# Performance work log

Measured on AMD Instinct MI355X. Metric: run time of the kernel, lower is better.

The kernel has to match this reference:

```python
import jax, jax.numpy as jnp
import numpy as np


def _forward(x, conv_w, conv_b, lin_w, lin_b, W_in, conv1d_w, conv1d_b, W_x, W_dt, b_dt, A_log, Dp, W_out, We, be, Wa, ba, Wq, bq):
    B, _, H, Wd = x.shape
    E = conv_w.shape[0]
    # conv stem: Conv2d(k=3, pad=1) -> flatten(2) -> Linear(H*W -> img_size)
    z = jax.lax.conv_general_dilated(x, conv_w, (1, 1), [(1, 1), (1, 1)],
                                     dimension_numbers=('NCHW', 'OIHW', 'NCHW'))
    z = z + conv_b[None, :, None, None]
    z = z.reshape(B, E, H * Wd)                              # [B,E,HW]
    z = jnp.einsum('ben,mn->bem', z, lin_w) + lin_b          # [B,E,L]
    u = z.transpose(2, 0, 1)                                 # [L,B,E]: Mamba sees batch=L, seq=B
    # ---- Mamba block (mamba_ssm reference math) ----
    di = W_in.shape[0] // 2
    xz = u @ W_in.T                                          # [L,seq,2*di]
    xm, zg = xz[..., :di], xz[..., di:]
    K = conv1d_w.shape[-1]
    xc = jax.lax.conv_general_dilated(xm.transpose(0, 2, 1), conv1d_w, (1,), [(K - 1, 0)],
                                      dimension_numbers=('NCH', 'OIH', 'NCH'),
                                      feature_group_count=di)  # causal depthwise conv
    xs = jax.nn.silu((xc + conv1d_b[None, :, None]).transpose(0, 2, 1))  # [L,seq,di]
    dbl = xs @ W_x.T                                         # [L,seq,dt_rank+2S]
    dt_rank = W_dt.shape[1]
    S = A_log.shape[1]
    delta = jax.nn.softplus(dbl[..., :dt_rank] @ W_dt.T + b_dt)          # [L,seq,di]
    Bm = dbl[..., dt_rank:dt_rank + S]                       # [L,seq,S]
    Cm = dbl[..., dt_rank + S:]                              # [L,seq,S]
    A = -jnp.exp(A_log)                                      # [di,S]

    def step(h, t):
        d_t, b_t, c_t, x_t = t                               # [L,di],[L,S],[L,S],[L,di]
        h = jnp.exp(d_t[:, :, None] * A) * h + (d_t * x_t)[:, :, None] * b_t[:, None, :]
        return h, jnp.einsum('lds,ls->ld', h, c_t)

    h0 = jnp.zeros((u.shape[0], di, S), xs.dtype)
    _, ys = jax.lax.scan(step, h0, (delta.transpose(1, 0, 2), Bm.transpose(1, 0, 2),
                                    Cm.transpose(1, 0, 2), xs.transpose(1, 0, 2)))
    y = (ys.transpose(1, 0, 2) + xs * Dp) * jax.nn.silu(zg)  # [L,seq,di]
    out = y @ W_out.T                                        # [L,seq,E]
    feat = out[-1]                                           # [B,E] (last 'mamba batch' row)
    return feat @ We.T + be, feat @ Wa.T + ba, feat @ Wq.T + bq


def setup_inputs() -> dict:
    key = jax.random.key(0)
    ks = jax.random.split(key, 16)
    B, C, IMG, E, S, K = 512, 1, 32, 128, 256, 4
    di, dt_rank = 2 * E, 8
    sc = 0.02
    return {
        'x': jax.random.normal(ks[0], (B, C, IMG, IMG), jnp.float32),
        'conv_w': sc * jax.random.normal(ks[1], (E, C, 3, 3), jnp.float32),
        'conv_b': jnp.zeros((E,), jnp.float32),
        'lin_w': sc * jax.random.normal(ks[2], (IMG, IMG * IMG), jnp.float32),
        'lin_b': jnp.zeros((IMG,), jnp.float32),
        'W_in': sc * jax.random.normal(ks[3], (2 * di, E), jnp.float32),
        'conv1d_w': sc * jax.random.normal(ks[4], (di, 1, K), jnp.float32),
        'conv1d_b': jnp.zeros((di,), jnp.float32),
        'W_x': sc * jax.random.normal(ks[5], (dt_rank + 2 * S, di), jnp.float32),
        'W_dt': sc * jax.random.normal(ks[6], (di, dt_rank), jnp.float32),
        'b_dt': 0.1 * jax.random.normal(ks[7], (di,), jnp.float32),
        'A_log': jnp.log(jnp.broadcast_to(jnp.arange(1, S + 1, dtype=jnp.float32), (di, S))),
        'Dp': jnp.ones((di,), jnp.float32),
        'W_out': sc * jax.random.normal(ks[8], (E, di), jnp.float32),
        'We': sc * jax.random.normal(ks[9], (1, E), jnp.float32),
        'be': jnp.zeros((1,), jnp.float32),
        'Wa': sc * jax.random.normal(ks[10], (3, E), jnp.float32),
        'ba': jnp.zeros((3,), jnp.float32),
        'Wq': sc * jax.random.normal(ks[11], (4, E), jnp.float32),
        'bq': jnp.zeros((4,), jnp.float32),
    }


def reference(x, conv_w, conv_b, lin_w, lin_b, W_in, conv1d_w, conv1d_b, W_x, W_dt, b_dt, A_log, Dp, W_out, We, be, Wa, ba, Wq, bq):
    return _forward(x, conv_w, conv_b, lin_w, lin_b, W_in, conv1d_w, conv1d_b, W_x,
                    W_dt, b_dt, A_log, Dp, W_out, We, be, Wa, ba, Wq, bq)
```

## Files before the change

kernel.cpp:

```cpp
#include <hip/hip_runtime.h>
#include <math.h>

#define BATCH 512
#define E     128
#define DI    256
#define S     256
#define DTR   8
#define KCONV 4
#define JWX   520

__device__ __forceinline__ float silu_f(float v) {
    return v / (1.0f + __expf(-v));
}

__global__ __launch_bounds__(256) void kT_transpose(
    const float* __restrict__ W_in, const float* __restrict__ W_x,
    const float* __restrict__ W_dt, const float* __restrict__ W_out,
    const float* __restrict__ c1w,
    float* __restrict__ W_inT, float* __restrict__ W_xT,
    float* __restrict__ W_dtT, float* __restrict__ W_outT,
    float* __restrict__ c1wT)
{
    const int bid = blockIdx.x;
    const float* src; float* dst; int J, K, j0;
    if (bid < 9)       { src = W_x;   dst = W_xT;   J = JWX; K = DI;  j0 = bid * 64; }
    else if (bid < 17) { src = W_in;  dst = W_inT;  J = 512; K = E;   j0 = (bid - 9) * 64; }
    else if (bid < 19) { src = W_out; dst = W_outT; J = E;   K = DI;  j0 = (bid - 17) * 64; }
    else if (bid < 23) { src = W_dt;  dst = W_dtT;  J = DI;  K = DTR; j0 = (bid - 19) * 64; }
    else               { src = c1w;   dst = c1wT;   J = DI;  K = KCONV; j0 = (bid - 23) * 64; }
    const int j = j0 + (threadIdx.x & 63);
    if (j >= J) return;
    for (int c = threadIdx.x >> 6; c < K; c += 4)
        dst[c * J + j] = src[j * K + c];
}

__global__ __launch_bounds__(256) void k1_conv_lin(
    const float* __restrict__ x, const float* __restrict__ conv_w,
    const float* __restrict__ conv_b, const float* __restrict__ lin_w,
    const float* __restrict__ lin_b, float* __restrict__ u31)
{
    const int b = blockIdx.x;
    const int tid = threadIdx.x;
    __shared__ float lw[1024];
    __shared__ float red[10][4];
    __shared__ float Tsh[10];

    const float4 lv = ((const float4*)(lin_w + 31 * 1024))[tid];
    ((float4*)lw)[tid] = lv;
    __syncthreads();

    float acc[10];
#pragma unroll
    for (int k = 0; k < 10; k++) acc[k] = 0.0f;

    const float4 xv = ((const float4*)(x + (size_t)b * 1024))[tid];
    const int p0 = tid * 4;
    const int h = p0 >> 5, w0 = p0 & 31;
    const float xa[4] = {xv.x, xv.y, xv.z, xv.w};
#pragma unroll
    for (int k = 0; k < 4; k++) {
        const float xval = xa[k];
        const int w = w0 + k;
#pragma unroll
        for (int i = 0; i < 3; i++) {
            const int hh = h - (i - 1);
            if (hh < 0 || hh > 31) continue;
#pragma unroll
            for (int j = 0; j < 3; j++) {
                const int ww = w - (j - 1);
                if (ww < 0 || ww > 31) continue;
                acc[i * 3 + j] += xval * lw[hh * 32 + ww];
            }
        }
    }
    acc[9] = lv.x + lv.y + lv.z + lv.w;

    const int wv = tid >> 6, ln = tid & 63;
#pragma unroll
    for (int k = 0; k < 10; k++) {
#pragma unroll
        for (int m = 1; m < 64; m <<= 1) acc[k] += __shfl_xor(acc[k], m, 64);
    }
    if (ln == 0) {
#pragma unroll
        for (int k = 0; k < 10; k++) red[k][wv] = acc[k];
    }
    __syncthreads();
    if (tid < 10) Tsh[tid] = red[tid][0] + red[tid][1] + red[tid][2] + red[tid][3];
    __syncthreads();

    if (tid < E) {
        const int e = tid;
        float v = lin_b[31] + conv_b[e] * Tsh[9];
#pragma unroll
        for (int k = 0; k < 9; k++) v += conv_w[e * 9 + k] * Tsh[k];
        u31[b * E + e] = v;
    }
}

__global__ __launch_bounds__(256) void k2a_win(
    const float* __restrict__ u31, const float* __restrict__ W_inT,
    float* __restrict__ xm, float* __restrict__ zg)
{
    const int bb = blockIdx.x * 4;
    const int tid = threadIdx.x;
    __shared__ float u[4][E];
    for (int i = tid; i < 4 * E; i += 256) u[i >> 7][i & 127] = u31[bb * E + i];
    __syncthreads();

    const int r = tid >> 6;
    const int j = blockIdx.y * 64 + (tid & 63);
    float a = 0.0f;
#pragma unroll 8
    for (int e = 0; e < E; e++) a += u[r][e] * W_inT[e * 512 + j];
    if (j < 256) xm[(bb + r) * DI + j] = a;
    else         zg[(bb + r) * DI + (j - 256)] = a;
}

__global__ __launch_bounds__(256) void k2b_conv_wx(
    const float* __restrict__ xm, const float* __restrict__ c1wT,
    const float* __restrict__ conv1d_b, const float* __restrict__ W_xT,
    const float* __restrict__ W_dtT, const float* __restrict__ b_dt,
    float* __restrict__ xs_g, float* __restrict__ delta_g,
    float* __restrict__ Bm, float* __restrict__ Cm)
{
    const int bb = blockIdx.x * 4;
    const int g = blockIdx.y;
    const int tid = threadIdx.x;
    __shared__ float xs[4][DI];
    __shared__ float dtin[4][8];

    for (int idx = tid; idx < 4 * DI; idx += 256) {
        const int r = idx >> 8, c = idx & 255;
        const int b = bb + r;
        float a = 0.0f;
#pragma unroll
        for (int k = 0; k < KCONV; k++) {
            const int src = b - 3 + k;
            if (src >= 0) a += xm[src * DI + c] * c1wT[k * DI + c];
        }
        a += conv1d_b[c];
        const float s = silu_f(a);
        xs[r][c] = s;
        if (g == 0) xs_g[b * DI + c] = s;
    }
    __syncthreads();

    const int r = tid >> 6;
    const int j = g * 64 + (tid & 63);
    if (j < JWX) {
        float a = 0.0f;
#pragma unroll 8
        for (int c = 0; c < DI; c++) a += xs[r][c] * W_xT[c * JWX + j];
        const int b = bb + r;
        if (j < DTR)          dtin[r][j] = a;
        else if (j < DTR + S) Bm[b * S + (j - DTR)] = a;
        else                  Cm[b * S + (j - DTR - S)] = a;
    }
    __syncthreads();

    if (g == 0) {
        const int d = tid;
        const float bd = b_dt[d];
#pragma unroll
        for (int r2 = 0; r2 < 4; r2++) {
            float a = bd;
#pragma unroll
            for (int q = 0; q < DTR; q++) a += dtin[r2][q] * W_dtT[q * DI + d];
            const float sp = (a > 20.0f) ? a : log1pf(__expf(a));
            delta_g[(bb + r2) * DI + d] = sp;
        }
    }
}

template <int NCv>
__global__ __launch_bounds__(256) void k3a_local(
    const float* __restrict__ A_log, const float* __restrict__ delta,
    const float* __restrict__ xs, const float* __restrict__ Bm,
    const float* __restrict__ Cm, float* __restrict__ y,
    float* __restrict__ hloc, float* __restrict__ Dchunk)
{
    constexpr int TCv = BATCH / NCv;
    const int tid = threadIdx.x;
    const int wv = tid >> 6, ln = tid & 63;
    const int d = blockIdx.x * 4 + wv;
    const int c = blockIdx.y;
    const int s0 = ln * 4;
    const int t0 = c * TCv;

    const float4 al = *(const float4*)(A_log + d * S + s0);
    float4 A;
    A.x = -__expf(al.x); A.y = -__expf(al.y);
    A.z = -__expf(al.z); A.w = -__expf(al.w);

    float4 h = make_float4(0.f, 0.f, 0.f, 0.f);
    float cd = 0.0f;
    float pr[8];

    for (int tb = 0; tb < TCv; tb += 8) {
#pragma unroll
        for (int i = 0; i < 8; i++) {
            const int tt = t0 + tb + i;
            const float dd = delta[tt * DI + d];
            cd += dd;
            const float u = dd * xs[tt * DI + d];
            const float4 B = *(const float4*)(Bm + tt * S + s0);
            const float4 C = *(const float4*)(Cm + tt * S + s0);
            h.x = __expf(dd * A.x) * h.x + u * B.x;
            h.y = __expf(dd * A.y) * h.y + u * B.y;
            h.z = __expf(dd * A.z) * h.z + u * B.z;
            h.w = __expf(dd * A.w) * h.w + u * B.w;
            pr[i] = h.x * C.x + h.y * C.y + h.z * C.z + h.w * C.w;
        }
#pragma unroll
        for (int i = 0; i < 8; i++) {
#pragma unroll
            for (int m = 1; m < 64; m <<= 1) pr[i] += __shfl_xor(pr[i], m, 64);
        }
        if (ln == 0) {
#pragma unroll
            for (int i = 0; i < 8; i++) y[(t0 + tb + i) * DI + d] = pr[i];
        }
    }

    *(float4*)(hloc + ((size_t)(c * DI + d)) * S + s0) = h;
    if (ln == 0) Dchunk[c * DI + d] = cd;
}

template <int NCv>
__global__ __launch_bounds__(256) void k3b_carry(
    const float* __restrict__ A_log, const float* __restrict__ hloc,
    const float* __restrict__ Dchunk, float* __restrict__ hin)
{
    const int d = blockIdx.x;
    const int s = threadIdx.x;
    const float A = -__expf(A_log[d * S + s]);

    float h = 0.0f;
    float hf = hloc[((size_t)(0 * DI + d)) * S + s];
    float Dc = Dchunk[0 * DI + d];
    for (int c = 1; c < NCv; c++) {
        float hf_n = 0.0f, Dc_n = 0.0f;
        if (c < NCv - 1) {
            hf_n = hloc[((size_t)(c * DI + d)) * S + s];
            Dc_n = Dchunk[c * DI + d];
        }
        h = hf + __expf(A * Dc) * h;
        hin[((size_t)(c * DI + d)) * S + s] = h;
        hf = hf_n; Dc = Dc_n;
    }
}

template <int NCv>
__global__ __launch_bounds__(256) void k3c_fix(
    const float* __restrict__ A_log, const float* __restrict__ delta,
    const float* __restrict__ Cm, const float* __restrict__ hin,
    float* __restrict__ y)
{
    constexpr int TCv = BATCH / NCv;
    const int tid = threadIdx.x;
    const int wv = tid >> 6, ln = tid & 63;
    const int d = blockIdx.x * 4 + wv;
    const int c = blockIdx.y + 1;
    const int s0 = ln * 4;
    const int t0 = c * TCv;

    const float4 al = *(const float4*)(A_log + d * S + s0);
    float4 A;
    A.x = -__expf(al.x); A.y = -__expf(al.y);
    A.z = -__expf(al.z); A.w = -__expf(al.w);

    const float4 hi = *(const float4*)(hin + ((size_t)(c * DI + d)) * S + s0);

    float cd = 0.0f;
    float pr[8];

    for (int tb = 0; tb < TCv; tb += 8) {
#pragma unroll
        for (int i = 0; i < 8; i++) {
            const int tt = t0 + tb + i;
            const float dd = delta[tt * DI + d];
            cd += dd;
            const float4 C = *(const float4*)(Cm + tt * S + s0);
            const float fx = hi.x * __expf(cd * A.x);
            const float fy = hi.y * __expf(cd * A.y);
            const float fz = hi.z * __expf(cd * A.z);
            const float fw = hi.w * __expf(cd * A.w);
            pr[i] = fx * C.x + fy * C.y + fz * C.z + fw * C.w;
        }
#pragma unroll
        for (int i = 0; i < 8; i++) {
#pragma unroll
            for (int m = 1; m < 64; m <<= 1) pr[i] += __shfl_xor(pr[i], m, 64);
        }
        if (ln == 0) {
#pragma unroll
            for (int i = 0; i < 8; i++) {
                const int tt = t0 + tb + i;
                y[tt * DI + d] += pr[i];
            }
        }
    }
}

__global__ __launch_bounds__(256) void k4_heads(
    const float* __restrict__ y, const float* __restrict__ xs,
    const float* __restrict__ Dp, const float* __restrict__ zg,
    const float* __restrict__ W_outT,
    const float* __restrict__ We, const float* __restrict__ be,
    const float* __restrict__ Wa, const float* __restrict__ ba,
    const float* __restrict__ Wq, const float* __restrict__ bq,
    float* __restrict__ out)
{
    const int bb = blockIdx.x * 2;
    const int tid = threadIdx.x;
    __shared__ float yf[2][DI];
    __shared__ float feat[2][E];

    for (int idx = tid; idx < 2 * DI; idx += 256) {
        const int r = idx >> 8, c = idx & 255;
        const int b = bb + r;
        const float z = zg[b * DI + c];
        yf[r][c] = (y[b * DI + c] + xs[b * DI + c] * Dp[c]) * silu_f(z);
    }
    __syncthreads();

    {
        const int r = tid >> 7, e = tid & 127;
        float a = 0.0f;
#pragma unroll 8
        for (int dd = 0; dd < DI; dd++) a += yf[r][dd] * W_outT[dd * E + e];
        feat[r][e] = a;
    }
    __syncthreads();

    if (tid < 16) {
        const int r = tid >> 3, hd = tid & 7;
        const int b = bb + r;
        const float* wrow;
        float bias;
        int dst;
        if (hd == 0)      { wrow = We;                 bias = be[0];      dst = b; }
        else if (hd < 4)  { wrow = Wa + (hd - 1) * E;  bias = ba[hd - 1]; dst = 512 + b * 3 + (hd - 1); }
        else              { wrow = Wq + (hd - 4) * E;  bias = bq[hd - 4]; dst = 2048 + b * 4 + (hd - 4); }
        float a = bias;
#pragma unroll 4
        for (int e = 0; e < E; e++) a += feat[r][e] * wrow[e];
        out[dst] = a;
    }
}

template <int NCv>
static void launch_scan(const float* A_log, const float* delta, const float* xs,
                        const float* Bm, const float* Cm, float* y,
                        float* hloc, float* hin, float* Dchunk, hipStream_t stream)
{
    k3a_local<NCv><<<dim3(64, NCv), 256, 0, stream>>>(A_log, delta, xs, Bm, Cm, y, hloc, Dchunk);
    k3b_carry<NCv><<<256, 256, 0, stream>>>(A_log, hloc, Dchunk, hin);
    k3c_fix<NCv><<<dim3(64, NCv - 1), 256, 0, stream>>>(A_log, delta, Cm, hin, y);
}

extern "C" void kernel_launch(void* const* d_in, const int* in_sizes, int n_in,
                              void* d_out, int out_size, void* d_ws, size_t ws_size,
                              hipStream_t stream)
{
    const float* x        = (const float*)d_in[0];
    const float* conv_w   = (const float*)d_in[1];
    const float* conv_b   = (const float*)d_in[2];
    const float* lin_w    = (const float*)d_in[3];
    const float* lin_b    = (const float*)d_in[4];
    const float* W_in     = (const float*)d_in[5];
    const float* conv1d_w = (const float*)d_in[6];
    const float* conv1d_b = (const float*)d_in[7];
    const float* W_x      = (const float*)d_in[8];
    const float* W_dt     = (const float*)d_in[9];
    const float* b_dt     = (const float*)d_in[10];
    const float* A_log    = (const float*)d_in[11];
    const float* Dp       = (const float*)d_in[12];
    const float* W_out    = (const float*)d_in[13];
    const float* We       = (const float*)d_in[14];
    const float* be       = (const float*)d_in[15];
    const float* Wa       = (const float*)d_in[16];
    const float* ba       = (const float*)d_in[17];
    const float* Wq       = (const float*)d_in[18];
    const float* bq       = (const float*)d_in[19];
    float* out = (float*)d_out;

    float* ws = (float*)d_ws;
    float* u31   = ws;
    float* xm    = u31 + 512 * 128;
    float* zg    = xm  + 512 * 256;
    float* xs    = zg  + 512 * 256;
    float* delta = xs  + 512 * 256;
    float* Bm    = delta + 512 * 256;
    float* Cm    = Bm  + 512 * 256;
    float* y     = Cm  + 512 * 256;
    float* W_inT = y   + 512 * 256;
    float* W_xT  = W_inT + 128 * 512;
    float* W_dtT = W_xT  + 256 * JWX;
    float* W_outT= W_dtT + 8 * 256;
    float* c1wT  = W_outT+ 256 * 128;
    float* tail  = c1wT  + 4 * 256;

    const size_t base_floats = (size_t)(tail - ws);

    kT_transpose<<<27, 256, 0, stream>>>(W_in, W_x, W_dt, W_out, conv1d_w,
                                         W_inT, W_xT, W_dtT, W_outT, c1wT);
    k1_conv_lin<<<512, 256, 0, stream>>>(x, conv_w, conv_b, lin_w, lin_b, u31);
    k2a_win<<<dim3(128, 8), 256, 0, stream>>>(u31, W_inT, xm, zg);
    k2b_conv_wx<<<dim3(128, 9), 256, 0, stream>>>(xm, c1wT, conv1d_b, W_xT, W_dtT, b_dt,
                                                  xs, delta, Bm, Cm);

    const size_t avail = ws_size / 4 - base_floats;
    if (avail >= (size_t)2 * 32 * DI * S + 32 * DI) {
        float* hloc = tail;
        float* hin  = hloc + (size_t)32 * DI * S;
        float* Dch  = hin  + (size_t)32 * DI * S;
        launch_scan<32>(A_log, delta, xs, Bm, Cm, y, hloc, hin, Dch, stream);
    } else if (avail >= (size_t)2 * 16 * DI * S + 16 * DI) {
        float* hloc = tail;
        float* hin  = hloc + (size_t)16 * DI * S;
        float* Dch  = hin  + (size_t)16 * DI * S;
        launch_scan<16>(A_log, delta, xs, Bm, Cm, y, hloc, hin, Dch, stream);
    } else {
        float* hloc = tail;
        float* hin  = hloc + (size_t)8 * DI * S;
        float* Dch  = hin  + (size_t)8 * DI * S;
        launch_scan<8>(A_log, delta, xs, Bm, Cm, y, hloc, hin, Dch, stream);
    }

    k4_heads<<<256, 256, 0, stream>>>(y, xs, Dp, zg, W_outT, We, be, Wa, ba, Wq, bq, out);
}
```

Before: 185.3 us.

## Fuse pre-kernels, merge W_in with conv/W_x, and fold carry scan into fix

Merges the weight-transpose and conv stem into one launch, and fuses the W_in projection with the causal conv and W_x projection into a single kernel. That kernel recomputes the three halo rows of xm in shared memory instead of writing xm to global. The separate inter-chunk carry kernel is removed; each fix block instead recomputes its incoming state by serially combining prior chunk states, so later chunks do redundant work. This cuts launch count and global traffic, but k2_fused now runs only 128 blocks, down from 1024 and 1152, which lowers parallelism.

```diff
diff --git a/kernel.cpp b/kernel.cpp
--- a/kernel.cpp
+++ b/kernel.cpp
@@ -13,7 +13,10 @@
     return v / (1.0f + __expf(-v));
 }
 
-__global__ __launch_bounds__(256) void kT_transpose(
+__global__ __launch_bounds__(256) void kA_pre(
+    const float* __restrict__ x, const float* __restrict__ conv_w,
+    const float* __restrict__ conv_b, const float* __restrict__ lin_w,
+    const float* __restrict__ lin_b, float* __restrict__ u31,
     const float* __restrict__ W_in, const float* __restrict__ W_x,
     const float* __restrict__ W_dt, const float* __restrict__ W_out,
     const float* __restrict__ c1w,
@@ -21,26 +24,23 @@
     float* __restrict__ W_dtT, float* __restrict__ W_outT,
     float* __restrict__ c1wT)
 {
-    const int bid = blockIdx.x;
-    const float* src; float* dst; int J, K, j0;
-    if (bid < 9)       { src = W_x;   dst = W_xT;   J = JWX; K = DI;  j0 = bid * 64; }
-    else if (bid < 17) { src = W_in;  dst = W_inT;  J = 512; K = E;   j0 = (bid - 9) * 64; }
-    else if (bid < 19) { src = W_out; dst = W_outT; J = E;   K = DI;  j0 = (bid - 17) * 64; }
-    else if (bid < 23) { src = W_dt;  dst = W_dtT;  J = DI;  K = DTR; j0 = (bid - 19) * 64; }
-    else               { src = c1w;   dst = c1wT;   J = DI;  K = KCONV; j0 = (bid - 23) * 64; }
-    const int j = j0 + (threadIdx.x & 63);
-    if (j >= J) return;
-    for (int c = threadIdx.x >> 6; c < K; c += 4)
-        dst[c * J + j] = src[j * K + c];
-}
-
-__global__ __launch_bounds__(256) void k1_conv_lin(
-    const float* __restrict__ x, const float* __restrict__ conv_w,
-    const float* __restrict__ conv_b, const float* __restrict__ lin_w,
-    const float* __restrict__ lin_b, float* __restrict__ u31)
-{
+    const int tid = threadIdx.x;
+    if (blockIdx.x >= 512) {
+        const int bid = blockIdx.x - 512;
+        const float* src; float* dst; int J, K, j0;
+        if (bid < 9)       { src = W_x;   dst = W_xT;   J = JWX; K = DI;    j0 = bid * 64; }
+        else if (bid < 17) { src = W_in;  dst = W_inT;  J = 512; K = E;     j0 = (bid - 9) * 64; }
+        else if (bid < 19) { src = W_out; dst = W_outT; J = E;   K = DI;    j0 = (bid - 17) * 64; }
+        else if (bid < 23) { src = W_dt;  dst = W_dtT;  J = DI;  K = DTR;   j0 = (bid - 19) * 64; }
+        else               { src = c1w;   dst = c1wT;   J = DI;  K = KCONV; j0 = (bid - 23) * 64; }
+        const int j = j0 + (tid & 63);
+        if (j >= J) return;
+        for (int c = tid >> 6; c < K; c += 4)
+            dst[c * J + j] = src[j * K + c];
+        return;
+    }
+
     const int b = blockIdx.x;
-    const int tid = threadIdx.x;
     __shared__ float lw[1024];
     __shared__ float red[10][4];
     __shared__ float Tsh[10];
@@ -98,77 +98,94 @@
     }
 }
 
-__global__ __launch_bounds__(256) void k2a_win(
+__global__ __launch_bounds__(256) void k2_fused(
     const float* __restrict__ u31, const float* __restrict__ W_inT,
-    float* __restrict__ xm, float* __restrict__ zg)
+    const float* __restrict__ c1wT, const float* __restrict__ conv1d_b,
+    const float* __restrict__ W_xT, const float* __restrict__ W_dtT,
+    const float* __restrict__ b_dt,
+    float* __restrict__ zg, float* __restrict__ xs_g,
+    float* __restrict__ delta_g, float* __restrict__ Bm, float* __restrict__ Cm)
 {
     const int bb = blockIdx.x * 4;
     const int tid = threadIdx.x;
-    __shared__ float u[4][E];
-    for (int i = tid; i < 4 * E; i += 256) u[i >> 7][i & 127] = u31[bb * E + i];
-    __syncthreads();
-
-    const int r = tid >> 6;
-    const int j = blockIdx.y * 64 + (tid & 63);
-    float a = 0.0f;
-#pragma unroll 8
-    for (int e = 0; e < E; e++) a += u[r][e] * W_inT[e * 512 + j];
-    if (j < 256) xm[(bb + r) * DI + j] = a;
-    else         zg[(bb + r) * DI + (j - 256)] = a;
-}
-
-__global__ __launch_bounds__(256) void k2b_conv_wx(
-    const float* __restrict__ xm, const float* __restrict__ c1wT,
-    const float* __restrict__ conv1d_b, const float* __restrict__ W_xT,
-    const float* __restrict__ W_dtT, const float* __restrict__ b_dt,
-    float* __restrict__ xs_g, float* __restrict__ delta_g,
-    float* __restrict__ Bm, float* __restrict__ Cm)
-{
-    const int bb = blockIdx.x * 4;
-    const int g = blockIdx.y;
-    const int tid = threadIdx.x;
-    __shared__ float xs[4][DI];
-    __shared__ float dtin[4][8];
+    __shared__ float u[7][E];
+    __shared__ float xmL[7][DI];
+    __shared__ float xsL[4][DI];
+    __shared__ float dt_in[4][8];
+
+    for (int idx = tid; idx < 7 * E; idx += 256) {
+        const int row = idx / E, e = idx - row * E;
+        const int b = bb - 3 + row;
+        u[row][e] = (b >= 0) ? u31[b * E + e] : 0.0f;
+    }
+    __syncthreads();
+
+    {
+        const int c = tid;
+        float xmAcc[7], zgAcc[4];
+#pragma unroll
+        for (int r = 0; r < 7; r++) xmAcc[r] = 0.0f;
+#pragma unroll
+        for (int r = 0; r < 4; r++) zgAcc[r] = 0.0f;
+#pragma unroll 4
+        for (int e = 0; e < E; e++) {
+            const float w0 = W_inT[e * 512 + c];
+            const float w1 = W_inT[e * 512 + 256 + c];
+#pragma unroll
+            for (int r = 0; r < 7; r++) xmAcc[r] += w0 * u[r][e];
+#pragma unroll
+            for (int r = 0; r < 4; r++) zgAcc[r] += w1 * u[3 + r][e];
+        }
+#pragma unroll
+        for (int r = 0; r < 7; r++) xmL[r][c] = xmAcc[r];
+#pragma unroll
+        for (int r = 0; r < 4; r++) zg[(bb + r) * DI + c] = zgAcc[r];
+    }
+    __syncthreads();
 
     for (int idx = tid; idx < 4 * DI; idx += 256) {
         const int r = idx >> 8, c = idx & 255;
-        const int b = bb + r;
         float a = 0.0f;
 #pragma unroll
-        for (int k = 0; k < KCONV; k++) {
-            const int src = b - 3 + k;
-            if (src >= 0) a += xm[src * DI + c] * c1wT[k * DI + c];
-        }
+        for (int k = 0; k < KCONV; k++)
+            a += xmL[r + k][c] * c1wT[k * DI + c];
         a += conv1d_b[c];
         const float s = silu_f(a);
-        xs[r][c] = s;
-        if (g == 0) xs_g[b * DI + c] = s;
-    }
-    __syncthreads();
-
-    const int r = tid >> 6;
-    const int j = g * 64 + (tid & 63);
-    if (j < JWX) {
-        float a = 0.0f;
-#pragma unroll 8
-        for (int c = 0; c < DI; c++) a += xs[r][c] * W_xT[c * JWX + j];
-        const int b = bb + r;
-        if (j < DTR)          dtin[r][j] = a;
-        else if (j < DTR + S) Bm[b * S + (j - DTR)] = a;
-        else                  Cm[b * S + (j - DTR - S)] = a;
-    }
-    __syncthreads();
-
-    if (g == 0) {
+        xsL[r][c] = s;
+        xs_g[(bb + r) * DI + c] = s;
+    }
+    __syncthreads();
+
+    for (int j = tid; j < JWX; j += 256) {
+        float acc[4];
+#pragma unroll
+        for (int r = 0; r < 4; r++) acc[r] = 0.0f;
+#pragma unroll 4
+        for (int c = 0; c < DI; c++) {
+            const float w = W_xT[c * JWX + j];
+#pragma unroll
+            for (int r = 0; r < 4; r++) acc[r] += w * xsL[r][c];
+        }
+#pragma unroll
+        for (int r = 0; r < 4; r++) {
+            const int b = bb + r;
+            if (j < DTR)          dt_in[r][j] = acc[r];
+            else if (j < DTR + S) Bm[b * S + (j - DTR)] = acc[r];
+            else                  Cm[b * S + (j - DTR - S)] = acc[r];
+        }
+    }
+    __syncthreads();
+
+    {
         const int d = tid;
         const float bd = b_dt[d];
 #pragma unroll
-        for (int r2 = 0; r2 < 4; r2++) {
+        for (int r = 0; r < 4; r++) {
             float a = bd;
 #pragma unroll
-            for (int q = 0; q < DTR; q++) a += dtin[r2][q] * W_dtT[q * DI + d];
+            for (int q = 0; q < DTR; q++) a += dt_in[r][q] * W_dtT[q * DI + d];
             const float sp = (a > 20.0f) ? a : log1pf(__expf(a));
-            delta_g[(bb + r2) * DI + d] = sp;
+            delta_g[(bb + r) * DI + d] = sp;
         }
     }
 }
@@ -228,34 +245,10 @@
 }
 
 template <int NCv>
-__global__ __launch_bounds__(256) void k3b_carry(
-    const float* __restrict__ A_log, const float* __restrict__ hloc,
-    const float* __restrict__ Dchunk, float* __restrict__ hin)
-{
-    const int d = blockIdx.x;
-    const int s = threadIdx.x;
-    const float A = -__expf(A_log[d * S + s]);
-
-    float h = 0.0f;
-    float hf = hloc[((size_t)(0 * DI + d)) * S + s];
-    float Dc = Dchunk[0 * DI + d];
-    for (int c = 1; c < NCv; c++) {
-        float hf_n = 0.0f, Dc_n = 0.0f;
-        if (c < NCv - 1) {
-            hf_n = hloc[((size_t)(c * DI + d)) * S + s];
-            Dc_n = Dchunk[c * DI + d];
-        }
-        h = hf + __expf(A * Dc) * h;
-        hin[((size_t)(c * DI + d)) * S + s] = h;
-        hf = hf_n; Dc = Dc_n;
-    }
-}
-
-template <int NCv>
 __global__ __launch_bounds__(256) void k3c_fix(
     const float* __restrict__ A_log, const float* __restrict__ delta,
-    const float* __restrict__ Cm, const float* __restrict__ hin,
-    float* __restrict__ y)
+    const float* __restrict__ Cm, const float* __restrict__ hloc,
+    const float* __restrict__ Dchunk, float* __restrict__ y)
 {
     constexpr int TCv = BATCH / NCv;
     const int tid = threadIdx.x;
@@ -270,7 +263,15 @@
     A.x = -__expf(al.x); A.y = -__expf(al.y);
     A.z = -__expf(al.z); A.w = -__expf(al.w);
 
-    const float4 hi = *(const float4*)(hin + ((size_t)(c * DI + d)) * S + s0);
+    float4 hi = make_float4(0.f, 0.f, 0.f, 0.f);
+    for (int cp = 1; cp <= c; cp++) {
+        const float4 hl = *(const float4*)(hloc + ((size_t)((cp - 1) * DI + d)) * S + s0);
+        const float Dc = Dchunk[(cp - 1) * DI + d];
+        hi.x = hl.x + __expf(A.x * Dc) * hi.x;
+        hi.y = hl.y + __expf(A.y * Dc) * hi.y;
+        hi.z = hl.z + __expf(A.z * Dc) * hi.z;
+        hi.w = hl.w + __expf(A.w * Dc) * hi.w;
+    }
 
     float cd = 0.0f;
     float pr[8];
@@ -353,11 +354,10 @@
 template <int NCv>
 static void launch_scan(const float* A_log, const float* delta, const float* xs,
                         const float* Bm, const float* Cm, float* y,
-                        float* hloc, float* hin, float* Dchunk, hipStream_t stream)
+                        float* hloc, float* Dchunk, hipStream_t stream)
 {
     k3a_local<NCv><<<dim3(64, NCv), 256, 0, stream>>>(A_log, delta, xs, Bm, Cm, y, hloc, Dchunk);
-    k3b_carry<NCv><<<256, 256, 0, stream>>>(A_log, hloc, Dchunk, hin);
-    k3c_fix<NCv><<<dim3(64, NCv - 1), 256, 0, stream>>>(A_log, delta, Cm, hin, y);
+    k3c_fix<NCv><<<dim3(64, NCv - 1), 256, 0, stream>>>(A_log, delta, Cm, hloc, Dchunk, y);
 }
 
 extern "C" void kernel_launch(void* const* d_in, const int* in_sizes, int n_in,
@@ -387,46 +387,41 @@
     float* out = (float*)d_out;
 
     float* ws = (float*)d_ws;
-    float* u31   = ws;
-    float* xm    = u31 + 512 * 128;
-    float* zg    = xm  + 512 * 256;
-    float* xs    = zg  + 512 * 256;
-    float* delta = xs  + 512 * 256;
-    float* Bm    = delta + 512 * 256;
-    float* Cm    = Bm  + 512 * 256;
-    float* y     = Cm  + 512 * 256;
-    float* W_inT = y   + 512 * 256;
-    float* W_xT  = W_inT + 128 * 512;
-    float* W_dtT = W_xT  + 256 * JWX;
-    float* W_outT= W_dtT + 8 * 256;
-    float* c1wT  = W_outT+ 256 * 128;
-    float* tail  = c1wT  + 4 * 256;
+    float* u31    = ws;
+    float* zg     = u31    + 512 * 128;
+    float* xs     = zg     + 512 * 256;
+    float* delta  = xs     + 512 * 256;
+    float* Bm     = delta  + 512 * 256;
+    float* Cm     = Bm     + 512 * 256;
+    float* y      = Cm     + 512 * 256;
+    float* W_inT  = y      + 512 * 256;
+    float* W_xT   = W_inT  + 128 * 512;
+    float* W_dtT  = W_xT   + 256 * JWX;
+    float* W_outT = W_dtT  + 8 * 256;
+    float* c1wT   = W_outT + 256 * 128;
+    float* tail   = c1wT   + 4 * 256;
 
     const size_t base_floats = (size_t)(tail - ws);
-
-    kT_transpose<<<27, 256, 0, stream>>>(W_in, W_x, W_dt, W_out, conv1d_w,
-                                         W_inT, W_xT, W_dtT, W_outT, c1wT);
-    k1_conv_lin<<<512, 256, 0, stream>>>(x, conv_w, conv_b, lin_w, lin_b, u31);
-    k2a_win<<<dim3(128, 8), 256, 0, stream>>>(u31, W_inT, xm, zg);
-    k2b_conv_wx<<<dim3(128, 9), 256, 0, stream>>>(xm, c1wT, conv1d_b, W_xT, W_dtT, b_dt,
-                                                  xs, delta, Bm, Cm);
-
     const size_t avail = ws_size / 4 - base_floats;
-    if (avail >= (size_t)2 * 32 * DI * S + 32 * DI) {
+
+    kA_pre<<<539, 256, 0, stream>>>(x, conv_w, conv_b, lin_w, lin_b, u31,
+                                    W_in, W_x, W_dt, W_out, conv1d_w,
+                                    W_inT, W_xT, W_dtT, W_outT, c1wT);
+    k2_fused<<<128, 256, 0, stream>>>(u31, W_inT, c1wT, conv1d_b, W_xT, W_dtT, b_dt,
+                                      zg, xs, delta, Bm, Cm);
+
+    if (avail >= (size_t)32 * DI * S + 32 * DI) {
         float* hloc = tail;
-        float* hin  = hloc + (size_t)32 * DI * S;
-        float* Dch  = hin  + (size_t)32 * DI * S;
-        launch_scan<32>(A_log, delta, xs, Bm, Cm, y, hloc, hin, Dch, stream);
-    } else if (avail >= (size_t)2 * 16 * DI * S + 16 * DI) {
+        float* Dch  = hloc + (size_t)32 * DI * S;
+        launch_scan<32>(A_log, delta, xs, Bm, Cm, y, hloc, Dch, stream);
+    } else if (avail >= (size_t)16 * DI * S + 16 * DI) {
         float* hloc = tail;
-        float* hin  = hloc + (size_t)16 * DI * S;
-        float* Dch  = hin  + (size_t)16 * DI * S;
-        launch_scan<16>(A_log, delta, xs, Bm, Cm, y, hloc, hin, Dch, stream);
+        float* Dch  = hloc + (size_t)16 * DI * S;
+        launch_scan<16>(A_log, delta, xs, Bm, Cm, y, hloc, Dch, stream);
     } else {
         float* hloc = tail;
-        float* hin  = hloc + (size_t)8 * DI * S;
-        float* Dch  = hin  + (size_t)8 * DI * S;
-        launch_scan<8>(A_log, delta, xs, Bm, Cm, y, hloc, hin, Dch, stream);
+        float* Dch  = hloc + (size_t)8 * DI * S;
+        launch_scan<8>(A_log, delta, xs, Bm, Cm, y, hloc, Dch, stream);
     }
 
     k4_heads<<<256, 256, 0, stream>>>(y, xs, Dp, zg, W_outT, We, be, Wa, ba, Wq, bq, out);
```

New measurement: 219.7 us. +18.6%, slower.
